# Optimization experiments

Measured on AMD Instinct MI355X. Metric: run time of the kernel, lower is better.

## Reference

```python
import jax, jax.numpy as jnp
import numpy as np

NQ = 6          # num_qubits
BS = 3          # basis_size (Pauli x,y,z)
HID = 32        # LSTM hidden size
SNAPS = 16      # max_num_snapshots
BATCH = 1024
DIM = 2 ** NQ   # 64


def _pauli():
    sx = np.array([[0., 1.], [1., 0.]], dtype=np.complex64)
    sy = np.array([[0., -1j], [1j, 0.]], dtype=np.complex64)
    sz = np.array([[1., 0.], [0., -1.]], dtype=np.complex64)
    return np.stack([sx, sy, sz], axis=0)


def setup_inputs():
    key = jax.random.key(0)
    ks = jax.random.split(key, 12)
    snapshot = jax.random.uniform(ks[0], (BATCH, NQ), jnp.float32, -1.0, 1.0)
    basis_comp_vector = jax.nn.softmax(
        jax.random.normal(ks[1], (BATCH, NQ, BS), jnp.float32), axis=-1)
    # valid density matrices: rho = A A^dag / tr
    ar = jax.random.normal(ks[2], (BATCH, DIM, DIM), jnp.float32)
    ai = jax.random.normal(ks[3], (BATCH, DIM, DIM), jnp.float32)
    A = ar + 1j * ai
    rho_c = jnp.einsum('bij,bkj->bik', A, jnp.conj(A))
    tr = jnp.trace(rho_c, axis1=1, axis2=2)[:, None, None]
    rho_c = rho_c / tr
    rho = jnp.stack([jnp.real(rho_c), jnp.imag(rho_c)], axis=1).astype(jnp.float32)
    h0 = jax.random.normal(ks[4], (BATCH, HID), jnp.float32)
    c0 = jax.random.normal(ks[5], (BATCH, HID), jnp.float32)
    in_dim = NQ + NQ * BS
    W_ih = jax.random.normal(ks[6], (4 * HID, in_dim), jnp.float32) * 0.1
    W_hh = jax.random.normal(ks[7], (4 * HID, HID), jnp.float32) * 0.1
    b_ih = jax.random.normal(ks[8], (4 * HID,), jnp.float32) * 0.05
    b_hh = jax.random.normal(ks[9], (4 * HID,), jnp.float32) * 0.05
    Wp = jax.random.normal(ks[10], (NQ, HID, BS), jnp.float32) * 0.1
    bp = jax.random.normal(ks[11], (NQ, BS), jnp.float32) * 0.05
    pauli = _pauli()
    basis_r = jnp.asarray(np.real(pauli), jnp.float32)
    basis_i = jnp.asarray(np.imag(pauli), jnp.float32)
    return {"snapshot": snapshot, "basis_comp_vector": basis_comp_vector,
            "rho": rho, "h0": h0, "c0": c0,
            "W_ih": W_ih, "W_hh": W_hh, "b_ih": b_ih, "b_hh": b_hh,
            "Wp": Wp, "bp": bp, "basis_r": basis_r, "basis_i": basis_i}


def _apply(p, M, axis, b):
    # apply 2x2 batched operator M [b,2,2] on tensor axis `axis` of p [b]+(2,)*2NQ
    pm = jnp.moveaxis(p, axis, 1)
    shp = pm.shape
    out = jnp.einsum('bij,bjr->bir', M, pm.reshape(b, 2, -1)).reshape(shp)
    return jnp.moveaxis(out, 1, axis)


def _measure(rho_t, probs, basis, basis_c, b):
    # sequential single-qubit measurement on the collapsing mixed state
    pc = probs.astype(jnp.complex64)
    M = jnp.einsum('bqs,sij->bqij', pc, basis)    # prob-mixed basis ops
    Mc = jnp.einsum('bqs,sij->bqij', pc, basis_c)
    p = rho_t
    outs = []
    for q in range(NQ):
        p = _apply(p, M[:, q], 1 + q, b)          # row index of qubit q
        p = _apply(p, Mc[:, q], 1 + NQ + q, b)    # col index of qubit q
        tr = jnp.trace(p.reshape(b, DIM, DIM), axis1=1, axis2=2)
        outs.append(jnp.real(tr))                 # measurement value s
        p = p / tr.reshape((b,) + (1,) * (2 * NQ))  # renormalized post-state
    return jnp.stack(outs, axis=1)                 # [b, NQ]


def _forward(snapshot, basis_comp_vector, rho, h0, c0,
             W_ih, W_hh, b_ih, b_hh, Wp, bp, basis_r, basis_i):
    b = snapshot.shape[0]
    basis = (basis_r + 1j * basis_i).astype(jnp.complex64)
    basis_c = jnp.conj(basis)
    rho_t = (rho[:, 0] + 1j * rho[:, 1]).astype(jnp.complex64)
    rho_t = rho_t.reshape((b,) + (2,) * (2 * NQ))

    x = jnp.concatenate([snapshot, basis_comp_vector.reshape(b, -1)], axis=-1)
    feats = [x]
    h, c = h0, c0
    for _ in range(SNAPS - 1):
        # torch LSTMCell: gate order i, f, g, o
        g = x @ W_ih.T + b_ih + h @ W_hh.T + b_hh
        gi, gf, gg, go = jnp.split(g, 4, axis=-1)
        c = jax.nn.sigmoid(gf) * c + jax.nn.sigmoid(gi) * jnp.tanh(gg)
        h = jax.nn.sigmoid(go) * jnp.tanh(c)
        probs = jax.nn.softmax(jnp.einsum('bh,qhs->bqs', h, Wp) + bp, axis=-1)
        # torch.Tensor(snapshot_batch) detaches -> stop_gradient
        snaps = jax.lax.stop_gradient(_measure(rho_t, probs, basis, basis_c, b))
        x = jnp.concatenate([snaps, probs.reshape(b, -1)], axis=-1)
        feats.append(x)

    # classical-shadow reconstruction: kron_q (I + 3 s_q B_q)/2, averaged
    eye2 = jnp.eye(2, dtype=jnp.complex64)
    acc = jnp.zeros((b, DIM, DIM), jnp.complex64)
    last_bv = None
    for xw in feats:
        shadow = xw[:, :NQ]
        bv = xw[:, NQ:].reshape(b, NQ, BS)
        last_bv = bv
        Bq = jnp.einsum('bqs,sij->bqij', bv.astype(jnp.complex64), basis)
        rc = (eye2 + 3.0 * shadow[:, :, None, None].astype(jnp.complex64) * Bq) / 2.0
        k = rc[:, 0]
        dd = 2
        for q in range(1, NQ):  # batched kron chain
            k = jnp.einsum('bij,bkl->bikjl', k, rc[:, q]).reshape(b, dd * 2, dd * 2)
            dd *= 2
        acc = acc + k
    rho_rec = acc / SNAPS
    out = jnp.stack([jnp.real(rho_rec), jnp.imag(rho_rec)], axis=1)
    return out, last_bv


def reference(snapshot, basis_comp_vector, rho, h0, c0,
              W_ih, W_hh, b_ih, b_hh, Wp, bp, basis_r, basis_i):
    return _forward(snapshot, basis_comp_vector, rho, h0, c0,
                    W_ih, W_hh, b_ih, b_hh, Wp, bp, basis_r, basis_i)
```

## Files before the change

kernel.cpp:

```cpp
#include <hip/hip_runtime.h>

#define NQ 6
#define HID 32
#define SNAPS 16
#define BATCH 1024
#define FSTRIDE 24
#define FTOT 384
#define KSTR 24
#define KF   192

typedef float vfloat4 __attribute__((ext_vector_type(4)));

__device__ __forceinline__ float sigm_f(float x) { return 1.0f / (1.0f + __expf(-x)); }
__device__ __forceinline__ float tanh_f(float x) { return 1.0f - 2.0f / (__expf(2.0f * x) + 1.0f); }

__device__ __forceinline__ void rc_entry(float g, float b0, float b1, float b2,
                                         int i, int j, float& re, float& im) {
    if (i == j) { re = 0.5f + (i ? -g * b2 : g * b2); im = 0.0f; }
    else        { re = g * b0;  im = (i ? g * b1 : -g * b1); }
}

__global__ __launch_bounds__(128, 2)
void lstm_kernel(const float* __restrict__ snapshot,
                 const float* __restrict__ bcv,
                 const float* __restrict__ h0,
                 const float* __restrict__ c0,
                 const float* __restrict__ W_ih,
                 const float* __restrict__ W_hh,
                 const float* __restrict__ b_ih,
                 const float* __restrict__ b_hh,
                 const float* __restrict__ Wp,
                 const float* __restrict__ bp,
                 float* __restrict__ feat_scratch,
                 float* __restrict__ out_tail)
{
    __shared__ __align__(16) float feat[FTOT];
    __shared__ __align__(16) float sh[HID];
    __shared__ __align__(16) float sg[128];

    const int b = blockIdx.x;
    const int t = threadIdx.x;

    float4 wih[6], whh[8];
    {
        const float4* p = (const float4*)(W_ih + t * 24);
        #pragma unroll
        for (int k = 0; k < 6; ++k) wih[k] = p[k];
        const float4* q = (const float4*)(W_hh + t * 32);
        #pragma unroll
        for (int k = 0; k < 8; ++k) whh[k] = q[k];
    }
    const float bias = b_ih[t] + b_hh[t];

    float wp[32];
    float bpv = 0.0f, c = 0.0f;
    if (t < 18) {
        int q = t / 3, s = t - 3 * q;
        #pragma unroll
        for (int k = 0; k < 32; ++k) wp[k] = Wp[q * 96 + 3 * k + s];
        bpv = bp[t];
    }
    if (t < 32) { c = c0[b * 32 + t]; sh[t] = h0[b * 32 + t]; }
    if (t < 24) feat[t] = (t < 6) ? snapshot[b * 6 + t] : bcv[b * 18 + (t - 6)];
    __syncthreads();

    for (int step = 0; step < SNAPS - 1; ++step) {
        {
            const float4* x4 = (const float4*)(feat + step * FSTRIDE);
            const float4* h4 = (const float4*)sh;
            float ga = bias, gb = 0.0f, gc = 0.0f, gd = 0.0f;
            #pragma unroll
            for (int k = 0; k < 6; ++k) {
                float4 xq = x4[k];
                ga += xq.x * wih[k].x + xq.y * wih[k].y;
                gb += xq.z * wih[k].z + xq.w * wih[k].w;
            }
            #pragma unroll
            for (int k = 0; k < 8; ++k) {
                float4 hq = h4[k];
                gc += hq.x * whh[k].x + hq.y * whh[k].y;
                gd += hq.z * whh[k].z + hq.w * whh[k].w;
            }
            sg[t] = (ga + gb) + (gc + gd);
        }
        __syncthreads();

        if (t < 64) {
            if (t < 32) {
                float gi = sg[t], gf = sg[32 + t], gg = sg[64 + t], go = sg[96 + t];
                c = sigm_f(gf) * c + sigm_f(gi) * tanh_f(gg);
                sh[t] = sigm_f(go) * tanh_f(c);
            }
            __builtin_amdgcn_wave_barrier();
            float lg0 = bpv, lg1 = 0.0f;
            const float4* h4b = (const float4*)sh;
            #pragma unroll
            for (int k = 0; k < 4; ++k) {
                float4 hq = h4b[k];
                lg0 += hq.x * wp[4 * k] + hq.y * wp[4 * k + 1]
                     + hq.z * wp[4 * k + 2] + hq.w * wp[4 * k + 3];
            }
            #pragma unroll
            for (int k = 4; k < 8; ++k) {
                float4 hq = h4b[k];
                lg1 += hq.x * wp[4 * k] + hq.y * wp[4 * k + 1]
                     + hq.z * wp[4 * k + 2] + hq.w * wp[4 * k + 3];
            }
            float logit = lg0 + lg1;
            int q3 = 3 * (t < 6 ? t : 0);
            float l0 = __shfl(logit, q3), l1 = __shfl(logit, q3 + 1), l2 = __shfl(logit, q3 + 2);
            if (t < 6) {
                float m = fmaxf(l0, fmaxf(l1, l2));
                float e0 = __expf(l0 - m), e1 = __expf(l1 - m), e2 = __expf(l2 - m);
                float inv = 1.0f / (e0 + e1 + e2);
                float p0 = e0 * inv, p1 = e1 * inv, p2 = e2 * inv;
                float snap = p0 * p0 + p1 * p1 + p2 * p2;
                float* fd = feat + (step + 1) * FSTRIDE;
                fd[t] = snap;
                fd[6 + 3 * t]     = p0;
                fd[6 + 3 * t + 1] = p1;
                fd[6 + 3 * t + 2] = p2;
            }
        }
        __syncthreads();
    }

    if (t < 96)
        ((float4*)(feat_scratch + (size_t)b * 8192))[t] = ((const float4*)feat)[t];
    if (t < 18) out_tail[b * 18 + t] = feat[15 * FSTRIDE + 6 + t];
}

__global__ __launch_bounds__(256, 4)
void recon_kernel(const float* feat_src,
                  float* out)
{
    __shared__ __align__(16) float sKA[16 * KF];
    __shared__ __align__(16) float sKB[16 * KF];
    __shared__ __align__(16) float feat[FTOT];

    const int b = blockIdx.x;
    const int t = threadIdx.x;

    if (t < 96)
        ((float4*)feat)[t] = ((const float4*)(feat_src + (size_t)b * 8192))[t];
    __syncthreads();

    for (int n = t; n < 2048; n += 256) {
        int f = n >> 7, r = n & 127;
        int half = r >> 6, a = r & 63;
        const float* fx = &feat[f * FSTRIDE];
        int i0 = (a >> 5) & 1, i1 = (a >> 4) & 1, i2 = (a >> 3) & 1;
        int j0 = (a >> 2) & 1, j1 = (a >> 1) & 1, j2 = a & 1;
        int q = 3 * half;
        float g0 = 1.5f * fx[q], g1 = 1.5f * fx[q + 1], g2 = 1.5f * fx[q + 2];
        const float* bb = fx + 6 + 3 * q;
        float r0, m0, r1, m1, r2, m2;
        rc_entry(g0, bb[0], bb[1], bb[2], i0, j0, r0, m0);
        rc_entry(g1, bb[3], bb[4], bb[5], i1, j1, r1, m1);
        rc_entry(g2, bb[6], bb[7], bb[8], i2, j2, r2, m2);
        float pr = r0 * r1 - m0 * m1, pi = r0 * m1 + m0 * r1;
        float qr = pr * r2 - pi * m2, qi = pr * m2 + pi * r2;
        int row = a >> 3, col = a & 7;
        if (half == 0) {
            int off = f * KF + col * KSTR + ((row & 1) ? (7 + row) : row);
            sKA[off] = qr; sKA[off + 1] = qi;
        } else {
            int off = f * KF + row * KSTR + 2 * col;
            sKB[off] = qr; sKB[off + 1] = qi;
        }
    }
    __syncthreads();

    const int u = t & 15, v = t >> 4;
    const float* baseA = sKA + (u >> 1) * KSTR + 8 * (v >> 3);
    const float* baseB = sKB + (v & 7) * KSTR + 8 * (u & 1);
    float accr[4][4], acci[4][4];
    #pragma unroll
    for (int e = 0; e < 4; ++e)
        #pragma unroll
        for (int d = 0; d < 4; ++d) { accr[e][d] = 0.0f; acci[e][d] = 0.0f; }

    #pragma unroll 2
    for (int f = 0; f < SNAPS; ++f) {
        float4 A0 = *(const float4*)(baseA + f * KF);
        float4 A1 = *(const float4*)(baseA + f * KF + 4);
        float4 B0 = *(const float4*)(baseB + f * KF);
        float4 B1 = *(const float4*)(baseB + f * KF + 4);
        float ar[4] = {A0.x, A0.z, A1.x, A1.z};
        float ai[4] = {A0.y, A0.w, A1.y, A1.w};
        float br[4] = {B0.x, B0.z, B1.x, B1.z};
        float bi[4] = {B0.y, B0.w, B1.y, B1.w};
        #pragma unroll
        for (int e = 0; e < 4; ++e)
            #pragma unroll
            for (int d = 0; d < 4; ++d) {
                accr[e][d] += ar[e] * br[d] - ai[e] * bi[d];
                acci[e][d] += ar[e] * bi[d] + ai[e] * br[d];
            }
    }

    const float s = 1.0f / 16.0f;
    float* outb = out + (size_t)b * 8192;
    #pragma unroll
    for (int e = 0; e < 4; ++e) {
        int i = v + 16 * e;
        vfloat4 r4 = { accr[e][0] * s, accr[e][1] * s, accr[e][2] * s, accr[e][3] * s };
        vfloat4 i4 = { acci[e][0] * s, acci[e][1] * s, acci[e][2] * s, acci[e][3] * s };
        __builtin_nontemporal_store(r4, (vfloat4*)(outb + i * 64 + 4 * u));
        __builtin_nontemporal_store(i4, (vfloat4*)(outb + 4096 + i * 64 + 4 * u));
    }
}

extern "C" void kernel_launch(void* const* d_in, const int* in_sizes, int n_in,
                              void* d_out, int out_size, void* d_ws, size_t ws_size,
                              hipStream_t stream) {
    const float* snapshot = (const float*)d_in[0];
    const float* bcv      = (const float*)d_in[1];
    const float* h0       = (const float*)d_in[3];
    const float* c0       = (const float*)d_in[4];
    const float* W_ih     = (const float*)d_in[5];
    const float* W_hh     = (const float*)d_in[6];
    const float* b_ih     = (const float*)d_in[7];
    const float* b_hh     = (const float*)d_in[8];
    const float* Wp       = (const float*)d_in[9];
    const float* bp       = (const float*)d_in[10];
    float* out = (float*)d_out;

    lstm_kernel<<<BATCH, 128, 0, stream>>>(
        snapshot, bcv, h0, c0, W_ih, W_hh, b_ih, b_hh, Wp, bp,
        out , out + (size_t)BATCH * 8192 );
    recon_kernel<<<BATCH, 256, 0, stream>>>(out, out);
}
```

Before: 135.1 us.

## Run LSTM recurrence in a single wavefront with register broadcasts via readlane

The LSTM kernel shrinks from 128 to 64 threads, so each lane computes two gate rows. Shared-memory gate and hidden buffers give way to register arrays filled with readlane broadcasts and shuffles. This removes both block-wide barriers per timestep from the serial 15-step recurrence. The cost is more registers per lane and 56 readlane operations per step to rebuild the hidden and input vectors.

```diff
diff --git a/kernel.cpp b/kernel.cpp
--- a/kernel.cpp
+++ b/kernel.cpp
@@ -14,13 +14,17 @@
 __device__ __forceinline__ float sigm_f(float x) { return 1.0f / (1.0f + __expf(-x)); }
 __device__ __forceinline__ float tanh_f(float x) { return 1.0f - 2.0f / (__expf(2.0f * x) + 1.0f); }
 
+__device__ __forceinline__ float rl(float v, int l) {
+    return __builtin_bit_cast(float, __builtin_amdgcn_readlane(__builtin_bit_cast(int, v), l));
+}
+
 __device__ __forceinline__ void rc_entry(float g, float b0, float b1, float b2,
                                          int i, int j, float& re, float& im) {
     if (i == j) { re = 0.5f + (i ? -g * b2 : g * b2); im = 0.0f; }
     else        { re = g * b0;  im = (i ? g * b1 : -g * b1); }
 }
 
-__global__ __launch_bounds__(128, 2)
+__global__ __launch_bounds__(64)
 void lstm_kernel(const float* __restrict__ snapshot,
                  const float* __restrict__ bcv,
                  const float* __restrict__ h0,
@@ -35,98 +39,115 @@
                  float* __restrict__ out_tail)
 {
     __shared__ __align__(16) float feat[FTOT];
-    __shared__ __align__(16) float sh[HID];
-    __shared__ __align__(16) float sg[128];
 
     const int b = blockIdx.x;
     const int t = threadIdx.x;
 
-    float4 wih[6], whh[8];
+    float4 wih0[6], wih1[6], whh0[8], whh1[8];
     {
-        const float4* p = (const float4*)(W_ih + t * 24);
-        #pragma unroll
-        for (int k = 0; k < 6; ++k) wih[k] = p[k];
-        const float4* q = (const float4*)(W_hh + t * 32);
-        #pragma unroll
-        for (int k = 0; k < 8; ++k) whh[k] = q[k];
-    }
-    const float bias = b_ih[t] + b_hh[t];
+        const float4* p0 = (const float4*)(W_ih + t * 24);
+        const float4* p1 = (const float4*)(W_ih + (t + 64) * 24);
+        #pragma unroll
+        for (int k = 0; k < 6; ++k) { wih0[k] = p0[k]; wih1[k] = p1[k]; }
+        const float4* q0 = (const float4*)(W_hh + t * 32);
+        const float4* q1 = (const float4*)(W_hh + (t + 64) * 32);
+        #pragma unroll
+        for (int k = 0; k < 8; ++k) { whh0[k] = q0[k]; whh1[k] = q1[k]; }
+    }
+    const float bias0 = b_ih[t] + b_hh[t];
+    const float bias1 = b_ih[t + 64] + b_hh[t + 64];
 
     float wp[32];
-    float bpv = 0.0f, c = 0.0f;
+    float bpv = 0.0f, cst = 0.0f;
     if (t < 18) {
         int q = t / 3, s = t - 3 * q;
         #pragma unroll
         for (int k = 0; k < 32; ++k) wp[k] = Wp[q * 96 + 3 * k + s];
         bpv = bp[t];
-    }
-    if (t < 32) { c = c0[b * 32 + t]; sh[t] = h0[b * 32 + t]; }
-    if (t < 24) feat[t] = (t < 6) ? snapshot[b * 6 + t] : bcv[b * 18 + (t - 6)];
-    __syncthreads();
+    } else {
+        #pragma unroll
+        for (int k = 0; k < 32; ++k) wp[k] = 0.0f;
+    }
+    if (t < 32) cst = c0[b * 32 + t];
+
+    float hval = (t < 32) ? h0[b * 32 + t] : 0.0f;
+    float shh[32], sx[24];
+    #pragma unroll
+    for (int k = 0; k < 32; ++k) shh[k] = rl(hval, k);
+
+    float x0v = 0.0f;
+    if (t < 24) x0v = (t < 6) ? snapshot[b * 6 + t] : bcv[b * 18 + (t - 6)];
+    if (t < 24) feat[t] = x0v;
+    #pragma unroll
+    for (int k = 0; k < 24; ++k) sx[k] = rl(x0v, k);
 
     for (int step = 0; step < SNAPS - 1; ++step) {
-        {
-            const float4* x4 = (const float4*)(feat + step * FSTRIDE);
-            const float4* h4 = (const float4*)sh;
-            float ga = bias, gb = 0.0f, gc = 0.0f, gd = 0.0f;
-            #pragma unroll
-            for (int k = 0; k < 6; ++k) {
-                float4 xq = x4[k];
-                ga += xq.x * wih[k].x + xq.y * wih[k].y;
-                gb += xq.z * wih[k].z + xq.w * wih[k].w;
-            }
-            #pragma unroll
-            for (int k = 0; k < 8; ++k) {
-                float4 hq = h4[k];
-                gc += hq.x * whh[k].x + hq.y * whh[k].y;
-                gd += hq.z * whh[k].z + hq.w * whh[k].w;
-            }
-            sg[t] = (ga + gb) + (gc + gd);
-        }
-        __syncthreads();
-
-        if (t < 64) {
-            if (t < 32) {
-                float gi = sg[t], gf = sg[32 + t], gg = sg[64 + t], go = sg[96 + t];
-                c = sigm_f(gf) * c + sigm_f(gi) * tanh_f(gg);
-                sh[t] = sigm_f(go) * tanh_f(c);
-            }
-            __builtin_amdgcn_wave_barrier();
-            float lg0 = bpv, lg1 = 0.0f;
-            const float4* h4b = (const float4*)sh;
-            #pragma unroll
-            for (int k = 0; k < 4; ++k) {
-                float4 hq = h4b[k];
-                lg0 += hq.x * wp[4 * k] + hq.y * wp[4 * k + 1]
-                     + hq.z * wp[4 * k + 2] + hq.w * wp[4 * k + 3];
-            }
-            #pragma unroll
-            for (int k = 4; k < 8; ++k) {
-                float4 hq = h4b[k];
-                lg1 += hq.x * wp[4 * k] + hq.y * wp[4 * k + 1]
-                     + hq.z * wp[4 * k + 2] + hq.w * wp[4 * k + 3];
-            }
-            float logit = lg0 + lg1;
-            int q3 = 3 * (t < 6 ? t : 0);
-            float l0 = __shfl(logit, q3), l1 = __shfl(logit, q3 + 1), l2 = __shfl(logit, q3 + 2);
-            if (t < 6) {
-                float m = fmaxf(l0, fmaxf(l1, l2));
-                float e0 = __expf(l0 - m), e1 = __expf(l1 - m), e2 = __expf(l2 - m);
-                float inv = 1.0f / (e0 + e1 + e2);
-                float p0 = e0 * inv, p1 = e1 * inv, p2 = e2 * inv;
-                float snap = p0 * p0 + p1 * p1 + p2 * p2;
-                float* fd = feat + (step + 1) * FSTRIDE;
-                fd[t] = snap;
-                fd[6 + 3 * t]     = p0;
-                fd[6 + 3 * t + 1] = p1;
-                fd[6 + 3 * t + 2] = p2;
-            }
-        }
-        __syncthreads();
-    }
-
-    if (t < 96)
-        ((float4*)(feat_scratch + (size_t)b * 8192))[t] = ((const float4*)feat)[t];
+        float a0 = bias0, a1 = 0.0f, a2 = bias1, a3 = 0.0f;
+        #pragma unroll
+        for (int k = 0; k < 6; ++k) {
+            a0 += sx[4 * k]     * wih0[k].x + sx[4 * k + 1] * wih0[k].y;
+            a1 += sx[4 * k + 2] * wih0[k].z + sx[4 * k + 3] * wih0[k].w;
+            a2 += sx[4 * k]     * wih1[k].x + sx[4 * k + 1] * wih1[k].y;
+            a3 += sx[4 * k + 2] * wih1[k].z + sx[4 * k + 3] * wih1[k].w;
+        }
+        float a4 = 0.0f, a5 = 0.0f, a6 = 0.0f, a7 = 0.0f;
+        #pragma unroll
+        for (int k = 0; k < 8; ++k) {
+            a4 += shh[4 * k]     * whh0[k].x + shh[4 * k + 1] * whh0[k].y;
+            a5 += shh[4 * k + 2] * whh0[k].z + shh[4 * k + 3] * whh0[k].w;
+            a6 += shh[4 * k]     * whh1[k].x + shh[4 * k + 1] * whh1[k].y;
+            a7 += shh[4 * k + 2] * whh1[k].z + shh[4 * k + 3] * whh1[k].w;
+        }
+        float g0 = (a0 + a1) + (a4 + a5);
+        float g1 = (a2 + a3) + (a6 + a7);
+
+        float gf = __shfl(g0, (t + 32) & 63);
+        float go = __shfl(g1, (t + 32) & 63);
+        float gi = g0, gg = g1;
+
+        cst = sigm_f(gf) * cst + sigm_f(gi) * tanh_f(gg);
+        hval = sigm_f(go) * tanh_f(cst);
+
+        #pragma unroll
+        for (int k = 0; k < 32; ++k) shh[k] = rl(hval, k);
+
+        float lg0 = bpv, lg1 = 0.0f;
+        #pragma unroll
+        for (int k = 0; k < 16; ++k) lg0 += shh[k] * wp[k];
+        #pragma unroll
+        for (int k = 16; k < 32; ++k) lg1 += shh[k] * wp[k];
+        float logit = lg0 + lg1;
+
+        int q3 = 3 * (t < 6 ? t : 0);
+        float l0 = __shfl(logit, q3), l1 = __shfl(logit, q3 + 1), l2 = __shfl(logit, q3 + 2);
+        float m = fmaxf(l0, fmaxf(l1, l2));
+        float e0 = __expf(l0 - m), e1 = __expf(l1 - m), e2 = __expf(l2 - m);
+        float inv = 1.0f / (e0 + e1 + e2);
+        float p0 = e0 * inv, p1 = e1 * inv, p2 = e2 * inv;
+        float snap = p0 * p0 + p1 * p1 + p2 * p2;
+
+        if (t < 6) {
+            float* fd = feat + (step + 1) * FSTRIDE;
+            fd[t] = snap;
+            fd[6 + 3 * t]     = p0;
+            fd[6 + 3 * t + 1] = p1;
+            fd[6 + 3 * t + 2] = p2;
+        }
+
+        #pragma unroll
+        for (int q = 0; q < 6; ++q) {
+            sx[q]          = rl(snap, q);
+            sx[6 + 3 * q]     = rl(p0, q);
+            sx[6 + 3 * q + 1] = rl(p1, q);
+            sx[6 + 3 * q + 2] = rl(p2, q);
+        }
+    }
+
+    __builtin_amdgcn_wave_barrier();
+    float4* dst = (float4*)(feat_scratch + (size_t)b * 8192);
+    const float4* srcf = (const float4*)feat;
+    dst[t] = srcf[t];
+    if (t < 32) dst[64 + t] = srcf[64 + t];
     if (t < 18) out_tail[b * 18 + t] = feat[15 * FSTRIDE + 6 + t];
 }
 
@@ -226,7 +247,7 @@
     const float* bp       = (const float*)d_in[10];
     float* out = (float*)d_out;
 
-    lstm_kernel<<<BATCH, 128, 0, stream>>>(
+    lstm_kernel<<<BATCH, 64, 0, stream>>>(
         snapshot, bcv, h0, c0, W_ih, W_hh, b_ih, b_hh, Wp, bp,
         out , out + (size_t)BATCH * 8192 );
     recon_kernel<<<BATCH, 256, 0, stream>>>(out, out);
```

Measured after the change: 133.2 us. Within noise of the previous version (-1.4%).
